# Kernel tuning notes

Measured on AMD Instinct MI355X. Metric: run time of the kernel, lower is better.

The kernel has to match this reference:

```python
import jax, jax.numpy as jnp
import numpy as np
from jax import lax

N = 2048
B = 8
CH = 10
START = 1
STOP = 65


def setup_inputs() -> dict:
    key = jax.random.key(0)
    ks = jax.random.split(key, 13)

    def g(k, s):
        return jax.random.normal(k, s, jnp.float32) * 0.05

    return {
        "x": jax.random.normal(ks[0], (B, 1, N, N), jnp.float32),
        "wl": g(ks[1], (CH // 2, 1, 3, N)), "bl": g(ks[2], (CH // 2,)),
        "wr": g(ks[3], (CH // 2, 1, N, 3)), "br": g(ks[4], (CH // 2,)),
        "wA": g(ks[5], (CH, CH, 3)), "bA": g(ks[6], (CH,)),
        "wB": g(ks[7], (CH, CH, 3)), "bB": g(ks[8], (CH,)),  # shared by layers 2&3 (torch list aliasing)
        "wT": g(ks[9], (CH, CH, 3)), "bT": g(ks[10], (CH,)),
        "wm": g(ks[11], (2, CH, 1)), "bm": g(ks[12], (2,)),
        "start": START, "stop": STOP,
    }


def _conv1d(h, w, b, pad):
    y = lax.conv_general_dilated(h, w, (1,), [(pad, pad)], dimension_numbers=("NCH", "OIH", "NCH"))
    return y + b[None, :, None]


def _forward(x, wl, bl, wr, br, wA, bA, wB, bB, wT, bT, wm, bm, start, stop):
    n = x.shape[-1]
    # scan_left: Conv2d kernel (3, n), padding (1, 0) -> (B, 5, n, 1) -> squeeze
    left_ = lax.conv_general_dilated(x, wl, (1, 1), [(1, 1), (0, 0)], dimension_numbers=("NCHW", "OIHW", "NCHW"))
    left_ = left_[..., 0] + bl[None, :, None]
    # scan_right: Conv2d kernel (n, 3), padding (0, 1) -> (B, 5, 1, n) -> squeeze
    right_ = lax.conv_general_dilated(x, wr, (1, 1), [(0, 0), (1, 1)], dimension_numbers=("NCHW", "OIHW", "NCHW"))
    right_ = right_[:, :, 0, :] + br[None, :, None]
    lr = jnp.concatenate([left_, right_], axis=1)  # (B, 10, n)
    h = jax.nn.relu(_conv1d(lr, wA, bA, 1))
    h = jax.nn.relu(_conv1d(h, wB, bB, 1))  # same weights twice: torch [conv, relu]*2 aliasing
    h = jax.nn.relu(_conv1d(h, wB, bB, 1))
    # ConvTranspose1d(k=3, stride=1, pad=1) == Conv1d with transposed, spatially-flipped kernel, pad=1
    wTc = jnp.flip(jnp.swapaxes(wT, 0, 1), -1)
    for _ in range(3):
        h = jax.nn.relu(_conv1d(h, wTc, bT, 1))
    m = jax.nn.sigmoid(_conv1d(h, wm, bm, 0))  # (B, 2, n)
    left, right = m[:, 0, :], m[:, 1, :]
    xs = x[:, 0]  # (B, n, n)
    preds = []
    for d in range(start, stop):  # static diagonal indices
        curr = jnp.exp(jnp.diagonal(xs, offset=d, axis1=1, axis2=2))  # (B, n-d)
        mass_in = curr[:, 1:] * right[:, 1:n - d] + curr[:, :-1] * left[:, d:n - 1]
        mass_out = right[:, 0:n - d - 1] + left[:, d + 1:n]
        p = jnp.log(mass_in / mass_out)
        preds.append(p - jnp.mean(p))  # scalar mean over batch+positions, as torch.mean
    return jnp.concatenate(preds, axis=1)  # ragged preds concatenated: (B, sum(n-d-1))


def reference(x, wl, bl, wr, br, wA, bA, wB, bB, wT, bT, wm, bm, start, stop):
    return _forward(x, wl, bl, wr, br, wA, bA, wB, bB, wT, bT, wm, bm, start, stop)
```

## Files before the change

### kernel.cpp

```cpp
#include <hip/hip_runtime.h>
#include <hip/hip_bf16.h>

#define NN 2048
#define BB 8
#define TROW 128928

typedef __attribute__((ext_vector_type(8))) short bf16x8;
typedef __attribute__((ext_vector_type(4))) unsigned u32x4;
typedef __attribute__((ext_vector_type(4))) float f32x4;

__device__ __forceinline__ unsigned pk2(float lo, float hi) {
    float2 t; t.x = lo; t.y = hi;
    __hip_bfloat162 h = __float22bfloat162_rn(t);
    union { __hip_bfloat162 h; unsigned u; } c; c.h = h;
    return c.u;
}

__device__ __forceinline__ float aload(const float* p) {
    return __hip_atomic_load(p, __ATOMIC_RELAXED, __HIP_MEMORY_SCOPE_AGENT);
}

__global__ __launch_bounds__(512, 2) void k_all(const float* __restrict__ x,
                                                const float* __restrict__ wl,
                                                const float* __restrict__ wr,
                                                const float* __restrict__ bl,
                                                const float* __restrict__ br,
                                                const float* __restrict__ wA, const float* __restrict__ bA,
                                                const float* __restrict__ wB, const float* __restrict__ bB,
                                                const float* __restrict__ wT, const float* __restrict__ bT,
                                                const float* __restrict__ wm, const float* __restrict__ bm,
                                                float* __restrict__ R,
                                                float* __restrict__ CSp,
                                                float* __restrict__ LEFT, float* __restrict__ RIGHT,
                                                float* __restrict__ psum,
                                                int* __restrict__ counters,
                                                float* __restrict__ outp) {
    __shared__ float T[65][65];
    __shared__ float buf0[10][80], buf1[10][80];
    __shared__ float W[3][10][10][3];
    __shared__ float Bs[3][10];
    __shared__ float Wm[2][10], Bm[2];
    __shared__ float psl[64];
    __shared__ float lfs[132], rts[68];

    const int tid = threadIdx.x;
    const int b   = blockIdx.x >> 5;
    const int rg  = blockIdx.x & 31;
    const int i0  = rg << 6;
    const int w   = tid >> 6;
    const int lane = tid & 63;

    if (tid < 256) {
        const int q = lane >> 4, m = lane & 15;
        const int r0 = i0 + w * 16;
        const int nrow = (m == 15) ? 14 : m;
        const float* ap = x + ((size_t)(b * NN + r0 + m)) * NN + q * 8;
        const float* bp = wl + (size_t)nrow * NN + q * 8;
        f32x4 acc = {0.f, 0.f, 0.f, 0.f};
#pragma unroll 4
        for (int it = 0; it < 64; it++) {
            const float* a0 = ap + it * 32;
            const float* b0 = bp + it * 32;
            float4 av0 = *(const float4*)(a0);
            float4 av1 = *(const float4*)(a0 + 4);
            float4 bv0 = *(const float4*)(b0);
            float4 bv1 = *(const float4*)(b0 + 4);
            union { bf16x8 v; u32x4 u; } A, Bv;
            A.u[0] = pk2(av0.x, av0.y); A.u[1] = pk2(av0.z, av0.w);
            A.u[2] = pk2(av1.x, av1.y); A.u[3] = pk2(av1.z, av1.w);
            Bv.u[0] = pk2(bv0.x, bv0.y); Bv.u[1] = pk2(bv0.z, bv0.w);
            Bv.u[2] = pk2(bv1.x, bv1.y); Bv.u[3] = pk2(bv1.z, bv1.w);
            acc = __builtin_amdgcn_mfma_f32_16x16x32_bf16(A.v, Bv.v, acc, 0, 0, 0);
        }
        float* rp = R + ((size_t)b * NN + r0) * 16;
#pragma unroll
        for (int reg = 0; reg < 4; reg++)
            rp[(q * 4 + reg) * 16 + m] = acc[reg];
    } else {
        const int t2 = tid - 256;
        const int rc = rg >> 1, jc = rg & 1;
        const int r0 = rc * 128;
        const int c0 = jc * 1024 + t2 * 4;
        const float* xp = x + ((size_t)b * NN + r0) * NN + c0;

        float acc[15][4];
#pragma unroll
        for (int k = 0; k < 15; k++)
#pragma unroll
            for (int e = 0; e < 4; e++) acc[k][e] = 0.f;

        for (int rb = 0; rb < 16; rb++) {
            float4 xv[8];
#pragma unroll
            for (int q = 0; q < 8; q++)
                xv[q] = *(const float4*)(xp + (size_t)(rb * 8 + q) * NN);
#pragma unroll
            for (int q = 0; q < 8; q++) {
                int h = r0 + rb * 8 + q;
#pragma unroll
                for (int k = 0; k < 15; k++) {
                    int c = k / 3, dw = k - c * 3;
                    float wk = wr[c * (NN * 3) + h * 3 + dw];
                    acc[k][0] = fmaf(xv[q].x, wk, acc[k][0]);
                    acc[k][1] = fmaf(xv[q].y, wk, acc[k][1]);
                    acc[k][2] = fmaf(xv[q].z, wk, acc[k][2]);
                    acc[k][3] = fmaf(xv[q].w, wk, acc[k][3]);
                }
            }
        }
        float* op = CSp + ((size_t)(rc * BB + b) * 16) * NN + c0;
#pragma unroll
        for (int k = 0; k < 15; k++) {
            float4 v; v.x = acc[k][0]; v.y = acc[k][1]; v.z = acc[k][2]; v.w = acc[k][3];
            *(float4*)(op + (size_t)k * NN) = v;
        }
    }
    __syncthreads();

    if (tid == 0) {
        __threadfence();
        atomicAdd(&counters[0], 1);
    }

    for (int idx = tid; idx < 900; idx += 512) {
        int set = idx / 300, rem = idx - set * 300;
        int o = rem / 30, rem2 = rem - o * 30, c = rem2 / 3, kk = rem2 - c * 3;
        float u;
        if (set == 0) u = wA[o * 30 + c * 3 + kk];
        else if (set == 1) u = wB[o * 30 + c * 3 + kk];
        else u = wT[c * 30 + o * 3 + (2 - kk)];
        W[set][o][c][kk] = u;
    }
    if (tid < 30) {
        float v = (tid < 10) ? bA[tid] : (tid < 20) ? bB[tid - 10] : bT[tid - 20];
        Bs[tid / 10][tid % 10] = v;
    }
    if (tid < 20) Wm[tid / 10][tid % 10] = wm[tid];
    if (tid < 2) Bm[tid] = bm[tid];

    for (int idx = tid; idx < 65 * 64; idx += 512) {
        int r = idx >> 6, dm1 = idx & 63;
        int row = i0 + r;
        int col = row + dm1 + 1;
        float v = 0.f;
        if (row < NN && col < NN) v = __expf(x[((size_t)b * NN + row) * NN + col]);
        T[r][dm1] = v;
    }

    if (tid == 0) {
        while (__hip_atomic_load(&counters[0], __ATOMIC_ACQUIRE, __HIP_MEMORY_SCOPE_AGENT) < 256) {
            __builtin_amdgcn_s_sleep(2);
        }
    }
    __syncthreads();

    for (int idx = tid; idx < 760; idx += 512) {
        int ch = idx / 76, p = idx - ch * 76;
        int g = i0 - 6 + p;
        float v = 0.f;
        if (g >= 0 && g < NN) {
            if (ch < 5) {
                v = bl[ch];
#pragma unroll
                for (int dh = 0; dh < 3; dh++) {
                    int r = g - 1 + dh;
                    if (r >= 0 && r < NN)
                        v += aload(&R[(size_t)(b * NN + r) * 16 + ch * 3 + dh]);
                }
            } else {
                int c = ch - 5;
                v = br[c];
#pragma unroll
                for (int dw = 0; dw < 3; dw++) {
                    int j = g - 1 + dw;
                    if (j >= 0 && j < NN) {
                        const float* base = CSp + ((size_t)b * 16 + c * 3 + dw) * NN + j;
                        float t[16];
#pragma unroll
                        for (int rc = 0; rc < 16; rc++)
                            t[rc] = aload(base + (size_t)rc * (8 * 16 * NN));
                        float s = 0.f;
#pragma unroll
                        for (int rc = 0; rc < 16; rc++) s += t[rc];
                        v += s;
                    }
                }
            }
        }
        buf0[ch][p] = v;
    }
    __syncthreads();

    float(*in)[80] = buf0;
    float(*out)[80] = buf1;
    for (int layer = 0; layer < 6; layer++) {
        int set = (layer == 0) ? 0 : (layer < 3 ? 1 : 2);
        int lo = layer + 1;
        for (int idx = tid; idx < 760; idx += 512) {
            int o = idx / 76, p = idx - o * 76;
            if (p >= lo && p < 76 - lo) {
                float s = Bs[set][o];
#pragma unroll
                for (int c = 0; c < 10; c++) {
                    const float* ip = &in[c][p];
                    s = fmaf(ip[-1], W[set][o][c][0], s);
                    s = fmaf(ip[0], W[set][o][c][1], s);
                    s = fmaf(ip[1], W[set][o][c][2], s);
                }
                s = s > 0.f ? s : 0.f;
                int g = i0 - 6 + p;
                if (g < 0 || g >= NN) s = 0.f;
                out[o][p] = s;
            }
        }
        __syncthreads();
        float(*tmp)[80] = in; in = out; out = tmp;
    }

    if (tid < 128) {
        int o = tid >> 6, pp = tid & 63;
        int p = 6 + pp;
        float s = Bm[o];
#pragma unroll
        for (int c = 0; c < 10; c++) s = fmaf(in[c][p], Wm[o][c], s);
        float sig = 1.f / (1.f + __expf(-s));
        float* dst = (o ? RIGHT : LEFT) + b * NN + i0 + pp;
        __hip_atomic_store(dst, sig, __ATOMIC_RELAXED, __HIP_MEMORY_SCOPE_AGENT);
    }
    __syncthreads();

    if (tid == 0) {
        __threadfence();
        atomicAdd(&counters[1], 1);
        while (__hip_atomic_load(&counters[1], __ATOMIC_ACQUIRE, __HIP_MEMORY_SCOPE_AGENT) < 256) {
            __builtin_amdgcn_s_sleep(2);
        }
    }
    __syncthreads();

    if (tid < 195) {
        if (tid < 129) {
            int g = i0 + 1 + tid; if (g > NN - 1) g = NN - 1;
            lfs[tid] = aload(LEFT + b * NN + g);
        } else {
            int p2 = tid - 129;
            int g = i0 + p2; if (g > NN - 1) g = NN - 1;
            rts[p2] = aload(RIGHT + b * NN + g);
        }
    }
    __syncthreads();

    int i = i0 + lane;
    float pv[8];
#pragma unroll
    for (int s = 0; s < 8; s++) {
        int dm1 = w * 8 + s;
        int d = dm1 + 1;
        int L = (NN - 1) - d;
        float p = 0.f;
        if (i < L) {
            float mi = T[lane + 1][dm1] * rts[lane + 1] + T[lane][dm1] * lfs[dm1 + lane];
            float mo = rts[lane] + lfs[dm1 + lane + 1];
            p = __logf(mi / mo);
        }
        pv[s] = p;
        float s64 = p;
        for (int off = 32; off; off >>= 1) s64 += __shfl_down(s64, off);
        if (lane == 0) psl[dm1] = s64;
    }
    __syncthreads();
    if (tid < 64) atomicAdd(&psum[tid], psl[tid]);
    __syncthreads();

    if (tid == 0) {
        __threadfence();
        atomicAdd(&counters[2], 1);
        while (__hip_atomic_load(&counters[2], __ATOMIC_ACQUIRE, __HIP_MEMORY_SCOPE_AGENT) < 256) {
            __builtin_amdgcn_s_sleep(2);
        }
    }
    __syncthreads();
    if (tid < 64)
        psl[tid] = aload(&psum[tid]);
    __syncthreads();

#pragma unroll
    for (int s = 0; s < 8; s++) {
        int dm1 = w * 8 + s;
        int d = dm1 + 1;
        int L = (NN - 1) - d;
        if (i < L) {
            float mean = psl[dm1] / (float)(8 * L);
            size_t off0 = (size_t)dm1 * (NN - 1) - (size_t)dm1 * (dm1 + 1) / 2;
            outp[(size_t)b * TROW + off0 + i] = pv[s] - mean;
        }
    }
}

extern "C" void kernel_launch(void* const* d_in, const int* in_sizes, int n_in,
                              void* d_out, int out_size, void* d_ws, size_t ws_size,
                              hipStream_t stream) {
    const float* x = (const float*)d_in[0];
    const float* wl = (const float*)d_in[1];
    const float* bl = (const float*)d_in[2];
    const float* wr = (const float*)d_in[3];
    const float* br = (const float*)d_in[4];
    const float* wA = (const float*)d_in[5];
    const float* bA = (const float*)d_in[6];
    const float* wB = (const float*)d_in[7];
    const float* bB = (const float*)d_in[8];
    const float* wT = (const float*)d_in[9];
    const float* bT = (const float*)d_in[10];
    const float* wm = (const float*)d_in[11];
    const float* bm = (const float*)d_in[12];

    float* ws = (float*)d_ws;
    float* R     = ws;
    float* CSp   = ws + 262144;
    float* LEFT  = ws + 4456448;
    float* RIGHT = ws + 4472832;
    float* psum  = ws + 4489216;
    int*   counters = (int*)(ws + 4489280);

    hipMemsetAsync(ws + 4489216, 0, (size_t)(64 + 4) * 4, stream);

    k_all<<<256, 512, 0, stream>>>(x, wl, wr, bl, br, wA, bA, wB, bB, wT, bT, wm, bm,
                                   R, CSp, LEFT, RIGHT, psum, counters, (float*)d_out);
}
```

Baseline: 303.8 us.

## Split reduction stage into separate kernel with more, smaller blocks

The first grid-wide phase (row-projection MFMA GEMV and column weighted sums) moves out of the fused persistent kernel into its own launch with 1024 blocks of 256 threads. The row reduction is split in two halves along K and the column reduction uses narrower column chunks, which gives more parallelism and occupancy across the GPU's compute units for the bandwidth-bound read of x. The first spin-barrier and the memset are dropped, since the kernel boundary now provides ordering and stage 1 zeroes the counters itself. The cost is a second launch and writing and reading twice as many partial sums in the workspace.

```diff
diff --git a/kernel.cpp b/kernel.cpp
--- a/kernel.cpp
+++ b/kernel.cpp
@@ -20,45 +20,34 @@
     return __hip_atomic_load(p, __ATOMIC_RELAXED, __HIP_MEMORY_SCOPE_AGENT);
 }
 
-__global__ __launch_bounds__(512, 2) void k_all(const float* __restrict__ x,
-                                                const float* __restrict__ wl,
-                                                const float* __restrict__ wr,
-                                                const float* __restrict__ bl,
-                                                const float* __restrict__ br,
-                                                const float* __restrict__ wA, const float* __restrict__ bA,
-                                                const float* __restrict__ wB, const float* __restrict__ bB,
-                                                const float* __restrict__ wT, const float* __restrict__ bT,
-                                                const float* __restrict__ wm, const float* __restrict__ bm,
-                                                float* __restrict__ R,
-                                                float* __restrict__ CSp,
-                                                float* __restrict__ LEFT, float* __restrict__ RIGHT,
-                                                float* __restrict__ psum,
-                                                int* __restrict__ counters,
-                                                float* __restrict__ outp) {
-    __shared__ float T[65][65];
-    __shared__ float buf0[10][80], buf1[10][80];
-    __shared__ float W[3][10][10][3];
-    __shared__ float Bs[3][10];
-    __shared__ float Wm[2][10], Bm[2];
-    __shared__ float psl[64];
-    __shared__ float lfs[132], rts[68];
-
-    const int tid = threadIdx.x;
-    const int b   = blockIdx.x >> 5;
-    const int rg  = blockIdx.x & 31;
-    const int i0  = rg << 6;
-    const int w   = tid >> 6;
-    const int lane = tid & 63;
-
-    if (tid < 256) {
-        const int q = lane >> 4, m = lane & 15;
-        const int r0 = i0 + w * 16;
-        const int nrow = (m == 15) ? 14 : m;
-        const float* ap = x + ((size_t)(b * NN + r0 + m)) * NN + q * 8;
-        const float* bp = wl + (size_t)nrow * NN + q * 8;
+__global__ __launch_bounds__(256, 4) void k_stage1(const float* __restrict__ x,
+                                                   const float* __restrict__ wl,
+                                                   const float* __restrict__ wr,
+                                                   float* __restrict__ Rp,
+                                                   float* __restrict__ CSp,
+                                                   float* __restrict__ psum,
+                                                   int* __restrict__ counters) {
+    int blk = blockIdx.x;
+    int tid = threadIdx.x;
+    if (blk == 0) {
+        if (tid < 64) psum[tid] = 0.f;
+        else if (tid < 68) counters[tid - 64] = 0;
+    }
+    if (blk < 512) {
+        int kh = blk & 1;
+        int unit = blk >> 1;
+        int b = unit >> 5, rg = unit & 31;
+        int w = tid >> 6, lane = tid & 63;
+        int q = lane >> 4, m = lane & 15;
+        int r0 = rg * 64 + w * 16;
+        int nrow = (m == 15) ? 14 : m;
+
+        const float* ap = x + ((size_t)(b * NN + r0 + m)) * NN + kh * 1024 + q * 8;
+        const float* bp = wl + (size_t)nrow * NN + kh * 1024 + q * 8;
+
         f32x4 acc = {0.f, 0.f, 0.f, 0.f};
 #pragma unroll 4
-        for (int it = 0; it < 64; it++) {
+        for (int it = 0; it < 32; it++) {
             const float* a0 = ap + it * 32;
             const float* b0 = bp + it * 32;
             float4 av0 = *(const float4*)(a0);
@@ -72,28 +61,28 @@
             Bv.u[2] = pk2(bv1.x, bv1.y); Bv.u[3] = pk2(bv1.z, bv1.w);
             acc = __builtin_amdgcn_mfma_f32_16x16x32_bf16(A.v, Bv.v, acc, 0, 0, 0);
         }
-        float* rp = R + ((size_t)b * NN + r0) * 16;
+        float* rp = Rp + (size_t)kh * (BB * NN * 16) + ((size_t)b * NN + r0) * 16;
 #pragma unroll
         for (int reg = 0; reg < 4; reg++)
             rp[(q * 4 + reg) * 16 + m] = acc[reg];
     } else {
-        const int t2 = tid - 256;
-        const int rc = rg >> 1, jc = rg & 1;
-        const int r0 = rc * 128;
-        const int c0 = jc * 1024 + t2 * 4;
+        int u2 = blk - 512;
+        int b = u2 >> 6;
+        int rem = u2 & 63;
+        int rc = rem >> 2, jc = rem & 3;
+        int r0 = rc * 128;
+        int c0 = jc * 512 + tid * 2;
         const float* xp = x + ((size_t)b * NN + r0) * NN + c0;
 
-        float acc[15][4];
-#pragma unroll
-        for (int k = 0; k < 15; k++)
-#pragma unroll
-            for (int e = 0; e < 4; e++) acc[k][e] = 0.f;
+        float acc[15][2];
+#pragma unroll
+        for (int k = 0; k < 15; k++) { acc[k][0] = 0.f; acc[k][1] = 0.f; }
 
         for (int rb = 0; rb < 16; rb++) {
-            float4 xv[8];
+            float2 xv[8];
 #pragma unroll
             for (int q = 0; q < 8; q++)
-                xv[q] = *(const float4*)(xp + (size_t)(rb * 8 + q) * NN);
+                xv[q] = *(const float2*)(xp + (size_t)(rb * 8 + q) * NN);
 #pragma unroll
             for (int q = 0; q < 8; q++) {
                 int h = r0 + rb * 8 + q;
@@ -103,24 +92,45 @@
                     float wk = wr[c * (NN * 3) + h * 3 + dw];
                     acc[k][0] = fmaf(xv[q].x, wk, acc[k][0]);
                     acc[k][1] = fmaf(xv[q].y, wk, acc[k][1]);
-                    acc[k][2] = fmaf(xv[q].z, wk, acc[k][2]);
-                    acc[k][3] = fmaf(xv[q].w, wk, acc[k][3]);
                 }
             }
         }
         float* op = CSp + ((size_t)(rc * BB + b) * 16) * NN + c0;
 #pragma unroll
         for (int k = 0; k < 15; k++) {
-            float4 v; v.x = acc[k][0]; v.y = acc[k][1]; v.z = acc[k][2]; v.w = acc[k][3];
-            *(float4*)(op + (size_t)k * NN) = v;
-        }
-    }
-    __syncthreads();
-
-    if (tid == 0) {
-        __threadfence();
-        atomicAdd(&counters[0], 1);
-    }
+            float2 v; v.x = acc[k][0]; v.y = acc[k][1];
+            *(float2*)(op + (size_t)k * NN) = v;
+        }
+    }
+}
+
+__global__ __launch_bounds__(512, 2) void k_rest(const float* __restrict__ x,
+                                                 const float* __restrict__ Rp,
+                                                 const float* __restrict__ CSp,
+                                                 const float* __restrict__ bl,
+                                                 const float* __restrict__ br,
+                                                 const float* __restrict__ wA, const float* __restrict__ bA,
+                                                 const float* __restrict__ wB, const float* __restrict__ bB,
+                                                 const float* __restrict__ wT, const float* __restrict__ bT,
+                                                 const float* __restrict__ wm, const float* __restrict__ bm,
+                                                 float* __restrict__ LEFT, float* __restrict__ RIGHT,
+                                                 float* __restrict__ psum,
+                                                 int* __restrict__ counters,
+                                                 float* __restrict__ outp) {
+    __shared__ float T[65][65];
+    __shared__ float buf0[10][80], buf1[10][80];
+    __shared__ float W[3][10][10][3];
+    __shared__ float Bs[3][10];
+    __shared__ float Wm[2][10], Bm[2];
+    __shared__ float psl[64];
+    __shared__ float lfs[132], rts[68];
+
+    const int tid = threadIdx.x;
+    const int b   = blockIdx.x >> 5;
+    const int rg  = blockIdx.x & 31;
+    const int i0  = rg << 6;
+    const int w   = tid >> 6;
+    const int lane = tid & 63;
 
     for (int idx = tid; idx < 900; idx += 512) {
         int set = idx / 300, rem = idx - set * 300;
@@ -147,13 +157,6 @@
         T[r][dm1] = v;
     }
 
-    if (tid == 0) {
-        while (__hip_atomic_load(&counters[0], __ATOMIC_ACQUIRE, __HIP_MEMORY_SCOPE_AGENT) < 256) {
-            __builtin_amdgcn_s_sleep(2);
-        }
-    }
-    __syncthreads();
-
     for (int idx = tid; idx < 760; idx += 512) {
         int ch = idx / 76, p = idx - ch * 76;
         int g = i0 - 6 + p;
@@ -164,8 +167,10 @@
 #pragma unroll
                 for (int dh = 0; dh < 3; dh++) {
                     int r = g - 1 + dh;
-                    if (r >= 0 && r < NN)
-                        v += aload(&R[(size_t)(b * NN + r) * 16 + ch * 3 + dh]);
+                    if (r >= 0 && r < NN) {
+                        const float* p0 = Rp + ((size_t)b * NN + r) * 16 + ch * 3 + dh;
+                        v += p0[0] + p0[(size_t)BB * NN * 16];
+                    }
                 }
             } else {
                 int c = ch - 5;
@@ -178,7 +183,7 @@
                         float t[16];
 #pragma unroll
                         for (int rc = 0; rc < 16; rc++)
-                            t[rc] = aload(base + (size_t)rc * (8 * 16 * NN));
+                            t[rc] = base[(size_t)rc * (8 * 16 * NN)];
                         float s = 0.f;
 #pragma unroll
                         for (int rc = 0; rc < 16; rc++) s += t[rc];
@@ -231,8 +236,8 @@
 
     if (tid == 0) {
         __threadfence();
-        atomicAdd(&counters[1], 1);
-        while (__hip_atomic_load(&counters[1], __ATOMIC_ACQUIRE, __HIP_MEMORY_SCOPE_AGENT) < 256) {
+        atomicAdd(&counters[0], 1);
+        while (__hip_atomic_load(&counters[0], __ATOMIC_ACQUIRE, __HIP_MEMORY_SCOPE_AGENT) < 256) {
             __builtin_amdgcn_s_sleep(2);
         }
     }
@@ -274,8 +279,8 @@
 
     if (tid == 0) {
         __threadfence();
-        atomicAdd(&counters[2], 1);
-        while (__hip_atomic_load(&counters[2], __ATOMIC_ACQUIRE, __HIP_MEMORY_SCOPE_AGENT) < 256) {
+        atomicAdd(&counters[1], 1);
+        while (__hip_atomic_load(&counters[1], __ATOMIC_ACQUIRE, __HIP_MEMORY_SCOPE_AGENT) < 256) {
             __builtin_amdgcn_s_sleep(2);
         }
     }
@@ -315,15 +320,14 @@
     const float* bm = (const float*)d_in[12];
 
     float* ws = (float*)d_ws;
-    float* R     = ws;
-    float* CSp   = ws + 262144;
-    float* LEFT  = ws + 4456448;
-    float* RIGHT = ws + 4472832;
-    float* psum  = ws + 4489216;
-    int*   counters = (int*)(ws + 4489280);
-
-    hipMemsetAsync(ws + 4489216, 0, (size_t)(64 + 4) * 4, stream);
-
-    k_all<<<256, 512, 0, stream>>>(x, wl, wr, bl, br, wA, bA, wB, bB, wT, bT, wm, bm,
-                                   R, CSp, LEFT, RIGHT, psum, counters, (float*)d_out);
-}
+    float* Rp    = ws;
+    float* CSp   = ws + 524288;
+    float* LEFT  = ws + 4718592;
+    float* RIGHT = ws + 4734976;
+    float* psum  = ws + 4751360;
+    int*   counters = (int*)(ws + 4751424);
+
+    k_stage1<<<1024, 256, 0, stream>>>(x, wl, wr, Rp, CSp, psum, counters);
+    k_rest<<<256, 512, 0, stream>>>(x, Rp, CSp, bl, br, wA, bA, wB, bB, wT, bT, wm, bm,
+                                    LEFT, RIGHT, psum, counters, (float*)d_out);
+}
```

Result: faster. 284.8 us (-6.3%).
